# Performance work log

Hardware: AMD Instinct MI355X
Metric: run time of the kernel (lower is better)

Reference implementation:

```python
import jax, jax.numpy as jnp
import numpy as np

CM = 0.05   # collision_margin
NT = 4      # n_timesteps

def _lin(x, W, b):
    return x @ W + b

def _mlp2(x, W1, b1, W2, b2):
    return _lin(jax.nn.relu(_lin(x, W1, b1)), W2, b2)

def _mlp3(x, W1, b1, W2, b2, W3, b3):
    h = jax.nn.relu(_lin(x, W1, b1))
    h = jax.nn.relu(_lin(h, W2, b2))
    return _lin(h, W3, b3)

def _xavier(key, fan_in, fan_out):
    std = np.sqrt(2.0 / (fan_in + fan_out))
    return jax.random.normal(key, (fan_in, fan_out), dtype=jnp.float32) * std

def setup_inputs() -> dict:
    key = jax.random.key(0)
    ks = jax.random.split(key, 16)
    sd, h, es, ud, rd, gd = 8, 128, 128, 32, 64, 32
    B, N, T = 16, 64, 8
    inp = {
        'states': jax.random.normal(ks[0], (B, N, T, sd), dtype=jnp.float32),
        'temp': 1,
        # StateEncoder: Linear(sd,h)-ReLU-Linear(h,es)-ReLU
        'sW1': _xavier(ks[1], sd, h), 'sb1': jnp.zeros((h,), jnp.float32),
        'sW2': _xavier(ks[2], h, es), 'sb2': jnp.zeros((es,), jnp.float32),
        # InputEncoder (collision_margin path): Linear(sd,h)-ReLU-Linear(h,ud)
        'uW1': _xavier(ks[3], sd, h), 'ub1': jnp.zeros((h,), jnp.float32),
        'uW2': _xavier(ks[4], h, ud), 'ub2': jnp.zeros((ud,), jnp.float32),
        # InputPropagator: Linear(es+ud, ud)
        'upW': _xavier(ks[5], es + ud, ud), 'upb': jnp.zeros((ud,), jnp.float32),
        # RelationEncoder (collision_margin path): Linear(sd,h)-ReLU-Linear(h,rd)
        'reW1': _xavier(ks[6], sd, h), 'reb1': jnp.zeros((h,), jnp.float32),
        'reW2': _xavier(ks[7], h, rd), 'reb2': jnp.zeros((rd,), jnp.float32),
        # RelationPropagator: Linear(2*es+rd, rd)
        'rpW': _xavier(ks[8], 2 * es + rd, rd), 'rpb': jnp.zeros((rd,), jnp.float32),
        # ComposedEmbedding: Linear(es+ud+rd,h)-ReLU-Linear(h,h)-ReLU-Linear(h,gd)
        'cW1': _xavier(ks[9], es + ud + rd, h), 'cb1': jnp.zeros((h,), jnp.float32),
        'cW2': _xavier(ks[10], h, h), 'cb2': jnp.zeros((h,), jnp.float32),
        'cW3': _xavier(ks[11], h, gd), 'cb3': jnp.zeros((gd,), jnp.float32),
    }
    return inp

def reference(states, temp, sW1, sb1, sW2, sb2, uW1, ub1, uW2, ub2, upW, upb,
              reW1, reb1, reW2, reb2, rpW, rpb, cW1, cb1, cW2, cb2, cW3, cb3):
    B, N, T, sd = states.shape
    BT = B * T
    s = states.transpose(0, 2, 1, 3).reshape(BT, N, sd)  # [BT,N,sd]

    # node encoders
    enc_obj = jax.nn.relu(_mlp2(s, sW1, sb1, sW2, sb2))   # [BT,N,es]
    enc_u = _mlp2(s, uW1, ub1, uW2, ub2)                  # [BT,N,ud] (no relu in collision_margin path)
    # u mask (get_u_states_mask)
    u = ((jnp.abs(s[..., 0:1]) > 1 - CM) | (jnp.abs(s[..., NT:NT + 1]) > 1 - CM)).astype(s.dtype)

    obs_u = jax.nn.relu(_lin(jnp.concatenate([enc_obj, enc_u], axis=-1), upW, upb))  # [BT,N,ud]
    enc_comp = jnp.concatenate([enc_obj, obs_u], axis=-1)  # [BT,N,es+ud]

    # pairwise relations: receiver i (dim1), sender j (dim2)
    rel_states = s[:, :, None, :] - s[:, None, :, :]        # [BT,N,N,sd]
    enc_rel = jax.nn.relu(_mlp2(rel_states, reW1, reb1, reW2, reb2))  # [BT,N,N,rd]
    sel = ((jnp.abs(rel_states[..., 0:1]) > 2 * CM) |
           (jnp.abs(rel_states[..., NT:NT + 1]) > 2 * CM)).astype(s.dtype)  # [BT,N,N,1]

    es = enc_obj.shape[-1]
    recv = jnp.broadcast_to(enc_obj[:, :, None, :], (BT, N, N, es))
    send = jnp.broadcast_to(enc_obj[:, None, :, :], (BT, N, N, es))
    rel_in = jnp.concatenate([recv, send, enc_rel], axis=-1)            # [BT,N,N,2es+rd]
    rel_eff = jax.nn.relu(_lin(rel_in, rpW, rpb)) * sel                 # [BT,N,N,rd]
    rel_agg = rel_eff.sum(axis=2)                                       # scatter-sum over senders -> [BT,N,rd]

    enc_comp = jnp.concatenate([enc_comp, rel_agg], axis=-1)            # [BT,N,es+ud+rd]
    g = _mlp3(enc_comp, cW1, cb1, cW2, cb2, cW3, cb3)                   # [BT,N,gd]
    return g.reshape(B, T, N, -1)
```

## Files before the change

### kernel.cpp

```cpp
#include <hip/hip_runtime.h>
#include <hip/hip_bf16.h>


typedef __bf16 bf16x8 __attribute__((ext_vector_type(8)));
typedef _Float16 half8 __attribute__((ext_vector_type(8)));
typedef float f32x4 __attribute__((ext_vector_type(4)));

static __device__ __forceinline__ half8 relu8(half8 x) {
    half8 z = {};
    return __builtin_elementwise_max(x, z);
}

__global__ __launch_bounds__(256) void k_prep(
    const float* __restrict__ sW1, const float* __restrict__ uW1,
    const float* __restrict__ reW1, const float* __restrict__ sW2,
    const float* __restrict__ uW2, const float* __restrict__ upW,
    const float* __restrict__ reW2, const float* __restrict__ rpW,
    const float* __restrict__ cW1, const float* __restrict__ cW2,
    const float* __restrict__ cW3,
    __bf16* __restrict__ Wl1f, __bf16* __restrict__ Ws2f,
    __bf16* __restrict__ Wu2f, __bf16* __restrict__ Wupf,
    __bf16* __restrict__ Wabf, _Float16* __restrict__ W2f,
    _Float16* __restrict__ Wbf, __bf16* __restrict__ Wc1f,
    __bf16* __restrict__ Wc2f, __bf16* __restrict__ Wc3f)
{
    const int tid  = blockIdx.x * 256 + threadIdx.x;
    const int nthr = gridDim.x * 256;

#define PACK(dst, CAST, NKT, NCT, EXPR)                             \
    for (int q = tid; q < (NKT) * (NCT) * 512; q += nthr) {         \
        const int f = q >> 9, rem = q & 511;                        \
        const int lane = rem >> 3, e = rem & 7;                     \
        const int kt = f / (NCT), ct = f % (NCT);                   \
        const int k = kt * 32 + (lane >> 4) * 8 + e;                \
        const int c = ct * 16 + (lane & 15);                        \
        (dst)[q] = (CAST)(EXPR);                                    \
        (void)k; (void)c;                                           \
    }

    PACK(Wl1f, __bf16, 1, 24, (k >= 8 ? 0.f :
        (c < 128 ? sW1[k * 128 + c] :
         c < 256 ? uW1[k * 128 + (c - 128)] : reW1[k * 128 + (c - 256)])))
    PACK(Ws2f, __bf16, 4, 8, sW2[k * 128 + c])
    PACK(Wu2f, __bf16, 4, 2, uW2[k * 32 + c])
    PACK(Wupf, __bf16, 5, 2, (k < 160 ? upW[k * 32 + c] : 0.f))
    PACK(Wabf, __bf16, 4, 8, (c < 64 ? rpW[k * 64 + c] : rpW[(128 + k) * 64 + (c - 64)]))
    PACK(W2f,  _Float16, 4, 4, reW2[k * 64 + c])
    PACK(Wbf,  _Float16, 2, 4, rpW[(256 + k) * 64 + c])
    PACK(Wc1f, __bf16, 7, 8, cW1[k * 128 + c])
    PACK(Wc2f, __bf16, 4, 8, cW2[k * 128 + c])
    PACK(Wc3f, __bf16, 4, 2, cW3[k * 32 + c])
#undef PACK
}

__global__ __launch_bounds__(512) void k_node(
    const float* __restrict__ states,
    const float* __restrict__ sb1, const float* __restrict__ sb2,
    const float* __restrict__ ub1, const float* __restrict__ ub2,
    const float* __restrict__ upb,
    const __bf16* __restrict__ Wl1f, const __bf16* __restrict__ Ws2f,
    const __bf16* __restrict__ Wu2f, const __bf16* __restrict__ Wupf,
    const __bf16* __restrict__ Wabf,
    _Float16* __restrict__ P_h, float* __restrict__ A_g,
    _Float16* __restrict__ Bh_g, __bf16* __restrict__ x_g)
{
    const int t = threadIdx.x;
    const int lane = t & 63;
    const int w = t >> 6;
    const int lr = lane >> 4, lc = lane & 15;
    const int nb = blockIdx.x * 16;

    __shared__ __bf16 s_h1hu[16 * 256];
    __shared__ __bf16 s_eoeu[16 * 192];

    bf16x8 af1 = {};
    if (lr == 0) {
        const int rg = nb + lc;
        const int bt = rg >> 6, n = rg & 63;
        const int b = bt >> 3, ts = bt & 7;
        const float* sp = &states[((size_t)((b * 64 + n) * 8 + ts)) * 8];
        const float4 s0 = *reinterpret_cast<const float4*>(sp);
        const float4 s1 = *reinterpret_cast<const float4*>(sp + 4);
        af1[0] = (__bf16)s0.x; af1[1] = (__bf16)s0.y;
        af1[2] = (__bf16)s0.z; af1[3] = (__bf16)s0.w;
        af1[4] = (__bf16)s1.x; af1[5] = (__bf16)s1.y;
        af1[6] = (__bf16)s1.z; af1[7] = (__bf16)s1.w;
    }

    #pragma unroll
    for (int ci = 0; ci < 3; ++ci) {
        const int ct = w * 3 + ci;
        const bf16x8 wf = *reinterpret_cast<const bf16x8*>(
            Wl1f + ((size_t)(ct * 64 + lane)) * 8);
        const float bias = (ct < 8) ? sb1[ct * 16 + lc]
                          : (ct < 16) ? ub1[(ct - 8) * 16 + lc] : 0.f;
        f32x4 acc = {bias, bias, bias, bias};
        acc = __builtin_amdgcn_mfma_f32_16x16x32_bf16(af1, wf, acc, 0, 0, 0);
        #pragma unroll
        for (int r = 0; r < 4; ++r) {
            const int jj = lr * 4 + r;
            if (ct < 16) {
                const int col = ct * 16 + lc;
                const int g = col >> 3;
                s_h1hu[jj * 256 + (((g ^ (jj & 7)) << 3) | (col & 7))] =
                    (__bf16)fmaxf(acc[r], 0.f);
            } else {
                P_h[(size_t)(nb + jj) * 128 + (ct - 16) * 16 + lc] =
                    (_Float16)acc[r];
            }
        }
    }
    __syncthreads();

    const int jr = lc;
    const int sw = lc & 7;
    bf16x8 h1f[4];
    #pragma unroll
    for (int kt = 0; kt < 4; ++kt)
        h1f[kt] = *reinterpret_cast<const bf16x8*>(
            &s_h1hu[jr * 256 + (((kt * 4 + lr) ^ sw) << 3)]);
    {
        const int ct = w;
        const float bias = sb2[ct * 16 + lc];
        f32x4 acc = {bias, bias, bias, bias};
        #pragma unroll
        for (int kt = 0; kt < 4; ++kt) {
            const bf16x8 wf = *reinterpret_cast<const bf16x8*>(
                Ws2f + ((size_t)((kt * 8 + ct) * 64 + lane)) * 8);
            acc = __builtin_amdgcn_mfma_f32_16x16x32_bf16(h1f[kt], wf, acc, 0, 0, 0);
        }
        #pragma unroll
        for (int r = 0; r < 4; ++r) {
            const int jj = lr * 4 + r;
            const int col = ct * 16 + lc;
            const __bf16 v = (__bf16)fmaxf(acc[r], 0.f);
            x_g[(size_t)(nb + jj) * 160 + col] = v;
            const int g = col >> 3;
            s_eoeu[jj * 192 + (((g ^ (jj & 7)) << 3) | (col & 7))] = v;
        }
    }
    if (w < 2) {
        bf16x8 huf[4];
        #pragma unroll
        for (int kt = 0; kt < 4; ++kt)
            huf[kt] = *reinterpret_cast<const bf16x8*>(
                &s_h1hu[jr * 256 + (((16 + kt * 4 + lr) ^ sw) << 3)]);
        const int ct = w;
        const float bias = ub2[ct * 16 + lc];
        f32x4 acc = {bias, bias, bias, bias};
        #pragma unroll
        for (int kt = 0; kt < 4; ++kt) {
            const bf16x8 wf = *reinterpret_cast<const bf16x8*>(
                Wu2f + ((size_t)((kt * 2 + ct) * 64 + lane)) * 8);
            acc = __builtin_amdgcn_mfma_f32_16x16x32_bf16(huf[kt], wf, acc, 0, 0, 0);
        }
        #pragma unroll
        for (int r = 0; r < 4; ++r) {
            const int jj = lr * 4 + r;
            const int col = 128 + ct * 16 + lc;
            const int g = col >> 3;
            s_eoeu[jj * 192 + (((g ^ (jj & 7)) << 3) | (col & 7))] = (__bf16)acc[r];
        }
    }
    __syncthreads();

    bf16x8 eof[5];
    #pragma unroll
    for (int kt = 0; kt < 4; ++kt)
        eof[kt] = *reinterpret_cast<const bf16x8*>(
            &s_eoeu[jr * 192 + (((kt * 4 + lr) ^ sw) << 3)]);
    eof[4] = *reinterpret_cast<const bf16x8*>(
        &s_eoeu[jr * 192 + (((16 + lr) ^ sw) << 3)]);

    if (w >= 6) {
        const int ct = w - 6;
        const float bias = upb[ct * 16 + lc];
        f32x4 acc = {bias, bias, bias, bias};
        #pragma unroll
        for (int kt = 0; kt < 5; ++kt) {
            const bf16x8 wf = *reinterpret_cast<const bf16x8*>(
                Wupf + ((size_t)((kt * 2 + ct) * 64 + lane)) * 8);
            acc = __builtin_amdgcn_mfma_f32_16x16x32_bf16(eof[kt], wf, acc, 0, 0, 0);
        }
        #pragma unroll
        for (int r = 0; r < 4; ++r) {
            const int rg = nb + lr * 4 + r;
            x_g[(size_t)rg * 160 + 128 + ct * 16 + lc] = (__bf16)fmaxf(acc[r], 0.f);
        }
    }
    {
        const int ct = w;
        f32x4 acc = {0.f, 0.f, 0.f, 0.f};
        #pragma unroll
        for (int kt = 0; kt < 4; ++kt) {
            const bf16x8 wf = *reinterpret_cast<const bf16x8*>(
                Wabf + ((size_t)((kt * 8 + ct) * 64 + lane)) * 8);
            acc = __builtin_amdgcn_mfma_f32_16x16x32_bf16(eof[kt], wf, acc, 0, 0, 0);
        }
        #pragma unroll
        for (int r = 0; r < 4; ++r) {
            const int rg = nb + lr * 4 + r;
            if (ct < 4) A_g[(size_t)rg * 64 + ct * 16 + lc] = acc[r];
            else        Bh_g[(size_t)rg * 64 + (ct - 4) * 16 + lc] = (_Float16)acc[r];
        }
    }
}

__global__ __launch_bounds__(512, 2) void k_pairc(
    const float* __restrict__ states,
    const _Float16* __restrict__ P_h, const float* __restrict__ A_g,
    const _Float16* __restrict__ Bh_g, const __bf16* __restrict__ x_g,
    const float* __restrict__ reb1, const float* __restrict__ reb2,
    const float* __restrict__ rpb,
    const _Float16* __restrict__ W2f, const _Float16* __restrict__ Wbf,
    const float* __restrict__ cb1, const float* __restrict__ cb2,
    const float* __restrict__ cb3,
    const __bf16* __restrict__ Wc1f, const __bf16* __restrict__ Wc2f,
    const __bf16* __restrict__ Wc3f,
    float* __restrict__ out)
{
    const int t    = threadIdx.x;
    const int lane = t & 63;
    const int w    = t >> 6;
    const int lr   = lane >> 4;
    const int lc   = lane & 15;
    const int bid  = (blockIdx.x & 7) * 64 + (blockIdx.x >> 3);
    const int bt   = bid >> 2;
    const int ig   = bid & 3;
    const int b    = bt >> 3, tstep = bt & 7;
    const int rowb = bt * 64 + ig * 16;

    __shared__ _Float16 s_pj[64 * 128];
    __shared__ _Float16 s_er[8][16 * 64];
    __shared__ _Float16 s_bm[64 * 72];
    __shared__ float    s_ai[16 * 64];
    __shared__ _Float16 s_rb[128];
    __shared__ float    s_s0[64], s_s4[64];

    for (int idx = t; idx < 1024; idx += 512) {
        const int j = idx >> 4, g = idx & 15;
        const half8 v = *reinterpret_cast<const half8*>(
            P_h + (size_t)(bt * 64 + j) * 128 + g * 8);
        *reinterpret_cast<half8*>(&s_pj[j * 128 + ((g ^ (j & 7)) << 3)]) = v;
    }
    {
        const int j = t >> 3, c8 = (t & 7) * 8;
        if (t < 512)
            *reinterpret_cast<half8*>(&s_bm[j * 72 + c8]) =
                *reinterpret_cast<const half8*>(
                    Bh_g + (size_t)(bt * 64 + j) * 64 + c8);
    }
    for (int idx = t; idx < 1024; idx += 512) {
        const int il = idx >> 6, c = idx & 63;
        s_ai[idx] = A_g[(size_t)(rowb + il) * 64 + c] + rpb[c];
    }
    if (t < 128) s_rb[t] = (_Float16)reb1[t];
    if (t < 64) {
        const float* sp = &states[((size_t)((b * 64 + t) * 8 + tstep)) * 8];
        s_s0[t] = sp[0];
        s_s4[t] = sp[4];
    }

    half8 w2f[4][4];
    #pragma unroll
    for (int kt = 0; kt < 4; ++kt)
        #pragma unroll
        for (int ct = 0; ct < 4; ++ct)
            w2f[kt][ct] = *reinterpret_cast<const half8*>(
                W2f + ((size_t)((kt * 4 + ct) * 64 + lane)) * 8);
    half8 wbf[2][4];
    #pragma unroll
    for (int kt = 0; kt < 2; ++kt)
        #pragma unroll
        for (int ct = 0; ct < 4; ++ct)
            wbf[kt][ct] = *reinterpret_cast<const half8*>(
                Wbf + ((size_t)((kt * 4 + ct) * 64 + lane)) * 8);
    float reb2c[4];
    #pragma unroll
    for (int ct = 0; ct < 4; ++ct) reb2c[ct] = reb2[ct * 16 + lc];

    __syncthreads();

    _Float16* er = s_er[w];
    float rag2[2][4];

    for (int q = 0; q < 2; ++q) {
        const int il = w * 2 + q;
        const int i  = ig * 16 + il;
        const int isw = i & 7;

        half8 pib[4];
        #pragma unroll
        for (int kt = 0; kt < 4; ++kt) {
            const int g = kt * 4 + lr;
            const half8 pv = *reinterpret_cast<const half8*>(
                &s_pj[i * 128 + ((g ^ isw) << 3)]);
            const half8 rb = *reinterpret_cast<const half8*>(&s_rb[g * 8]);
            pib[kt] = pv + rb;
        }
        float aic[4];
        #pragma unroll
        for (int ct = 0; ct < 4; ++ct) aic[ct] = s_ai[il * 64 + ct * 16 + lc];
        const unsigned long long selm = __ballot(
            fabsf(s_s0[i] - s_s0[lane]) > 0.1f ||
            fabsf(s_s4[i] - s_s4[lane]) > 0.1f);

        float ragg[4] = {0.f, 0.f, 0.f, 0.f};

        for (int jt = 0; jt < 4; ++jt) {
            const int j = jt * 16 + lc;
            const int jsw = j & 7;
            half8 af[4];
            #pragma unroll
            for (int kt = 0; kt < 4; ++kt) {
                const int g = (kt * 4 + lr) ^ jsw;
                const half8 pj = *reinterpret_cast<const half8*>(
                    &s_pj[j * 128 + (g << 3)]);
                af[kt] = relu8(pib[kt] - pj);
            }
            #pragma unroll
            for (int ct = 0; ct < 4; ++ct) {
                f32x4 acc = {reb2c[ct], reb2c[ct], reb2c[ct], reb2c[ct]};
                #pragma unroll
                for (int kt = 0; kt < 4; ++kt)
                    acc = __builtin_amdgcn_mfma_f32_16x16x32_f16(
                        af[kt], w2f[kt][ct], acc, 0, 0, 0);
                #pragma unroll
                for (int r = 0; r < 4; ++r) {
                    const int jj2 = lr * 4 + r;
                    const int c = ct * 16 + lc;
                    er[jj2 * 64 + ((((c >> 3) ^ (jj2 & 7)) << 3) | (c & 7))] =
                        (_Float16)fmaxf(acc[r], 0.f);
                }
            }
            half8 a2[2];
            #pragma unroll
            for (int kt = 0; kt < 2; ++kt) {
                const int g = (kt * 4 + lr) ^ (lc & 7);
                a2[kt] = *reinterpret_cast<const half8*>(&er[lc * 64 + (g << 3)]);
            }
            #pragma unroll
            for (int ct = 0; ct < 4; ++ct) {
                f32x4 acc = {aic[ct], aic[ct], aic[ct], aic[ct]};
                #pragma unroll
                for (int kt = 0; kt < 2; ++kt)
                    acc = __builtin_amdgcn_mfma_f32_16x16x32_f16(
                        a2[kt], wbf[kt][ct], acc, 0, 0, 0);
                #pragma unroll
                for (int r = 0; r < 4; ++r) {
                    const int jj = jt * 16 + lr * 4 + r;
                    const float bm = (float)s_bm[jj * 72 + ct * 16 + lc];
                    float v = fmaxf(acc[r] + bm, 0.f);
                    v = ((selm >> jj) & 1ull) ? v : 0.f;
                    ragg[ct] += v;
                }
            }
        }
        #pragma unroll
        for (int ct = 0; ct < 4; ++ct) {
            ragg[ct] += __shfl_xor(ragg[ct], 16);
            ragg[ct] += __shfl_xor(ragg[ct], 32);
            rag2[q][ct] = ragg[ct];
        }
    }
    __syncthreads();

    __bf16* s_x  = reinterpret_cast<__bf16*>(s_pj);
    __bf16* s_h1 = s_x + 16 * 256;
    __bf16* s_h2 = s_h1 + 16 * 128;

    for (int idx = t; idx < 320; idx += 512) {
        const int j = idx / 20, g = idx - j * 20;
        const bf16x8 v = *reinterpret_cast<const bf16x8*>(
            x_g + (size_t)(rowb + j) * 160 + g * 8);
        *reinterpret_cast<bf16x8*>(&s_x[j * 256 + ((g ^ (j & 7)) << 3)]) = v;
    }
    if (lr == 0) {
        #pragma unroll
        for (int q = 0; q < 2; ++q) {
            const int il = w * 2 + q;
            #pragma unroll
            for (int ct = 0; ct < 4; ++ct) {
                const int c = ct * 16 + lc;
                const int gg = 20 + (c >> 3);
                s_x[il * 256 + ((gg ^ (il & 7)) << 3) + (c & 7)] =
                    (__bf16)rag2[q][ct];
            }
        }
    }
    __syncthreads();

    const int jr = lc;
    const int sw = lc & 7;
    bf16x8 xf[7];
    #pragma unroll
    for (int kt = 0; kt < 7; ++kt)
        xf[kt] = *reinterpret_cast<const bf16x8*>(
            &s_x[jr * 256 + (((kt * 4 + lr) ^ sw) << 3)]);
    {
        const int ct = w;
        const float bias = cb1[ct * 16 + lc];
        f32x4 acc = {bias, bias, bias, bias};
        #pragma unroll
        for (int kt = 0; kt < 7; ++kt) {
            const bf16x8 wf = *reinterpret_cast<const bf16x8*>(
                Wc1f + ((size_t)((kt * 8 + ct) * 64 + lane)) * 8);
            acc = __builtin_amdgcn_mfma_f32_16x16x32_bf16(xf[kt], wf, acc, 0, 0, 0);
        }
        #pragma unroll
        for (int r = 0; r < 4; ++r) {
            const int jj = lr * 4 + r;
            const int col = ct * 16 + lc, g = col >> 3;
            s_h1[jj * 128 + (((g ^ (jj & 7)) << 3) | (col & 7))] =
                (__bf16)fmaxf(acc[r], 0.f);
        }
    }
    __syncthreads();

    bf16x8 hf[4];
    #pragma unroll
    for (int kt = 0; kt < 4; ++kt)
        hf[kt] = *reinterpret_cast<const bf16x8*>(
            &s_h1[jr * 128 + (((kt * 4 + lr) ^ sw) << 3)]);
    {
        const int ct = w;
        const float bias = cb2[ct * 16 + lc];
        f32x4 acc = {bias, bias, bias, bias};
        #pragma unroll
        for (int kt = 0; kt < 4; ++kt) {
            const bf16x8 wf = *reinterpret_cast<const bf16x8*>(
                Wc2f + ((size_t)((kt * 8 + ct) * 64 + lane)) * 8);
            acc = __builtin_amdgcn_mfma_f32_16x16x32_bf16(hf[kt], wf, acc, 0, 0, 0);
        }
        #pragma unroll
        for (int r = 0; r < 4; ++r) {
            const int jj = lr * 4 + r;
            const int col = ct * 16 + lc, g = col >> 3;
            s_h2[jj * 128 + (((g ^ (jj & 7)) << 3) | (col & 7))] =
                (__bf16)fmaxf(acc[r], 0.f);
        }
    }
    __syncthreads();

    if (w < 2) {
        bf16x8 h2f[4];
        #pragma unroll
        for (int kt = 0; kt < 4; ++kt)
            h2f[kt] = *reinterpret_cast<const bf16x8*>(
                &s_h2[jr * 128 + (((kt * 4 + lr) ^ sw) << 3)]);
        const int ct = w;
        const float bias = cb3[ct * 16 + lc];
        f32x4 acc = {bias, bias, bias, bias};
        #pragma unroll
        for (int kt = 0; kt < 4; ++kt) {
            const bf16x8 wf = *reinterpret_cast<const bf16x8*>(
                Wc3f + ((size_t)((kt * 2 + ct) * 64 + lane)) * 8);
            acc = __builtin_amdgcn_mfma_f32_16x16x32_bf16(h2f[kt], wf, acc, 0, 0, 0);
        }
        #pragma unroll
        for (int r = 0; r < 4; ++r) {
            const int rg = rowb + lr * 4 + r;
            out[(size_t)rg * 32 + ct * 16 + lc] = acc[r];
        }
    }
}

extern "C" void kernel_launch(void* const* d_in, const int* in_sizes, int n_in,
                              void* d_out, int out_size, void* d_ws, size_t ws_size,
                              hipStream_t stream) {
    const float* states = (const float*)d_in[0];
    const float* sW1  = (const float*)d_in[2];
    const float* sb1  = (const float*)d_in[3];
    const float* sW2  = (const float*)d_in[4];
    const float* sb2  = (const float*)d_in[5];
    const float* uW1  = (const float*)d_in[6];
    const float* ub1  = (const float*)d_in[7];
    const float* uW2  = (const float*)d_in[8];
    const float* ub2  = (const float*)d_in[9];
    const float* upW  = (const float*)d_in[10];
    const float* upb  = (const float*)d_in[11];
    const float* reW1 = (const float*)d_in[12];
    const float* reb1 = (const float*)d_in[13];
    const float* reW2 = (const float*)d_in[14];
    const float* reb2 = (const float*)d_in[15];
    const float* rpW  = (const float*)d_in[16];
    const float* rpb  = (const float*)d_in[17];
    const float* cW1  = (const float*)d_in[18];
    const float* cb1  = (const float*)d_in[19];
    const float* cW2  = (const float*)d_in[20];
    const float* cb2  = (const float*)d_in[21];
    const float* cW3  = (const float*)d_in[22];
    const float* cb3  = (const float*)d_in[23];
    float* out = (float*)d_out;

    float* ws = (float*)d_ws;
    float* A_g = ws;
    _Float16* P_h  = (_Float16*)(A_g + 8192 * 64);
    _Float16* Bh_g = P_h + 8192 * 128;
    _Float16* W2f  = Bh_g + 8192 * 64;
    _Float16* Wbf  = W2f + 16 * 512;
    __bf16* x_g  = (__bf16*)(Wbf + 8 * 512);
    __bf16* Wl1f = x_g + 8192 * 160;
    __bf16* Ws2f = Wl1f + 24 * 512;
    __bf16* Wu2f = Ws2f + 32 * 512;
    __bf16* Wupf = Wu2f + 8 * 512;
    __bf16* Wabf = Wupf + 10 * 512;
    __bf16* Wc1f = Wabf + 32 * 512;
    __bf16* Wc2f = Wc1f + 56 * 512;
    __bf16* Wc3f = Wc2f + 32 * 512;

    k_prep<<<64, 256, 0, stream>>>(sW1, uW1, reW1, sW2, uW2, upW, reW2, rpW,
                                   cW1, cW2, cW3,
                                   Wl1f, Ws2f, Wu2f, Wupf, Wabf, W2f, Wbf,
                                   Wc1f, Wc2f, Wc3f);
    k_node<<<512, 512, 0, stream>>>(states, sb1, sb2, ub1, ub2, upb,
                                    Wl1f, Ws2f, Wu2f, Wupf, Wabf,
                                    P_h, A_g, Bh_g, x_g);
    k_pairc<<<512, 512, 0, stream>>>(states, P_h, A_g, Bh_g, x_g,
                                     reb1, reb2, rpb, W2f, Wbf,
                                     cb1, cb2, cb3, Wc1f, Wc2f, Wc3f, out);
}
```

Measured before the change: 147.2 us.

## Fuse node-encoder kernel into pairwise kernel, recomputing per-timestep node features

Merges k_node into the pairwise/composition kernel. Each block now computes the state encoder, the first relation-layer projection (P) and the sender projection (B) for all 64 nodes of its timestep in shared memory, instead of reading them from global workspace. This removes a kernel launch and the global round trip for P_h, A_g, Bh_g and x_g. The cost is redundant work: each of the four blocks sharing a timestep recomputes the node encoder for all 64 nodes. Shared memory use also rises, which may limit occupancy under launch_bounds(512,2).

```diff
diff --git a/kernel.cpp b/kernel.cpp
--- a/kernel.cpp
+++ b/kernel.cpp
@@ -4,6 +4,7 @@
 
 typedef __bf16 bf16x8 __attribute__((ext_vector_type(8)));
 typedef _Float16 half8 __attribute__((ext_vector_type(8)));
+typedef _Float16 half4 __attribute__((ext_vector_type(4)));
 typedef float f32x4 __attribute__((ext_vector_type(4)));
 
 static __device__ __forceinline__ half8 relu8(half8 x) {
@@ -53,168 +54,18 @@
 #undef PACK
 }
 
-__global__ __launch_bounds__(512) void k_node(
+__global__ __launch_bounds__(512, 2) void k_mega(
     const float* __restrict__ states,
     const float* __restrict__ sb1, const float* __restrict__ sb2,
     const float* __restrict__ ub1, const float* __restrict__ ub2,
-    const float* __restrict__ upb,
+    const float* __restrict__ upb, const float* __restrict__ reb1,
+    const float* __restrict__ reb2, const float* __restrict__ rpb,
+    const float* __restrict__ cb1, const float* __restrict__ cb2,
+    const float* __restrict__ cb3,
     const __bf16* __restrict__ Wl1f, const __bf16* __restrict__ Ws2f,
     const __bf16* __restrict__ Wu2f, const __bf16* __restrict__ Wupf,
     const __bf16* __restrict__ Wabf,
-    _Float16* __restrict__ P_h, float* __restrict__ A_g,
-    _Float16* __restrict__ Bh_g, __bf16* __restrict__ x_g)
-{
-    const int t = threadIdx.x;
-    const int lane = t & 63;
-    const int w = t >> 6;
-    const int lr = lane >> 4, lc = lane & 15;
-    const int nb = blockIdx.x * 16;
-
-    __shared__ __bf16 s_h1hu[16 * 256];
-    __shared__ __bf16 s_eoeu[16 * 192];
-
-    bf16x8 af1 = {};
-    if (lr == 0) {
-        const int rg = nb + lc;
-        const int bt = rg >> 6, n = rg & 63;
-        const int b = bt >> 3, ts = bt & 7;
-        const float* sp = &states[((size_t)((b * 64 + n) * 8 + ts)) * 8];
-        const float4 s0 = *reinterpret_cast<const float4*>(sp);
-        const float4 s1 = *reinterpret_cast<const float4*>(sp + 4);
-        af1[0] = (__bf16)s0.x; af1[1] = (__bf16)s0.y;
-        af1[2] = (__bf16)s0.z; af1[3] = (__bf16)s0.w;
-        af1[4] = (__bf16)s1.x; af1[5] = (__bf16)s1.y;
-        af1[6] = (__bf16)s1.z; af1[7] = (__bf16)s1.w;
-    }
-
-    #pragma unroll
-    for (int ci = 0; ci < 3; ++ci) {
-        const int ct = w * 3 + ci;
-        const bf16x8 wf = *reinterpret_cast<const bf16x8*>(
-            Wl1f + ((size_t)(ct * 64 + lane)) * 8);
-        const float bias = (ct < 8) ? sb1[ct * 16 + lc]
-                          : (ct < 16) ? ub1[(ct - 8) * 16 + lc] : 0.f;
-        f32x4 acc = {bias, bias, bias, bias};
-        acc = __builtin_amdgcn_mfma_f32_16x16x32_bf16(af1, wf, acc, 0, 0, 0);
-        #pragma unroll
-        for (int r = 0; r < 4; ++r) {
-            const int jj = lr * 4 + r;
-            if (ct < 16) {
-                const int col = ct * 16 + lc;
-                const int g = col >> 3;
-                s_h1hu[jj * 256 + (((g ^ (jj & 7)) << 3) | (col & 7))] =
-                    (__bf16)fmaxf(acc[r], 0.f);
-            } else {
-                P_h[(size_t)(nb + jj) * 128 + (ct - 16) * 16 + lc] =
-                    (_Float16)acc[r];
-            }
-        }
-    }
-    __syncthreads();
-
-    const int jr = lc;
-    const int sw = lc & 7;
-    bf16x8 h1f[4];
-    #pragma unroll
-    for (int kt = 0; kt < 4; ++kt)
-        h1f[kt] = *reinterpret_cast<const bf16x8*>(
-            &s_h1hu[jr * 256 + (((kt * 4 + lr) ^ sw) << 3)]);
-    {
-        const int ct = w;
-        const float bias = sb2[ct * 16 + lc];
-        f32x4 acc = {bias, bias, bias, bias};
-        #pragma unroll
-        for (int kt = 0; kt < 4; ++kt) {
-            const bf16x8 wf = *reinterpret_cast<const bf16x8*>(
-                Ws2f + ((size_t)((kt * 8 + ct) * 64 + lane)) * 8);
-            acc = __builtin_amdgcn_mfma_f32_16x16x32_bf16(h1f[kt], wf, acc, 0, 0, 0);
-        }
-        #pragma unroll
-        for (int r = 0; r < 4; ++r) {
-            const int jj = lr * 4 + r;
-            const int col = ct * 16 + lc;
-            const __bf16 v = (__bf16)fmaxf(acc[r], 0.f);
-            x_g[(size_t)(nb + jj) * 160 + col] = v;
-            const int g = col >> 3;
-            s_eoeu[jj * 192 + (((g ^ (jj & 7)) << 3) | (col & 7))] = v;
-        }
-    }
-    if (w < 2) {
-        bf16x8 huf[4];
-        #pragma unroll
-        for (int kt = 0; kt < 4; ++kt)
-            huf[kt] = *reinterpret_cast<const bf16x8*>(
-                &s_h1hu[jr * 256 + (((16 + kt * 4 + lr) ^ sw) << 3)]);
-        const int ct = w;
-        const float bias = ub2[ct * 16 + lc];
-        f32x4 acc = {bias, bias, bias, bias};
-        #pragma unroll
-        for (int kt = 0; kt < 4; ++kt) {
-            const bf16x8 wf = *reinterpret_cast<const bf16x8*>(
-                Wu2f + ((size_t)((kt * 2 + ct) * 64 + lane)) * 8);
-            acc = __builtin_amdgcn_mfma_f32_16x16x32_bf16(huf[kt], wf, acc, 0, 0, 0);
-        }
-        #pragma unroll
-        for (int r = 0; r < 4; ++r) {
-            const int jj = lr * 4 + r;
-            const int col = 128 + ct * 16 + lc;
-            const int g = col >> 3;
-            s_eoeu[jj * 192 + (((g ^ (jj & 7)) << 3) | (col & 7))] = (__bf16)acc[r];
-        }
-    }
-    __syncthreads();
-
-    bf16x8 eof[5];
-    #pragma unroll
-    for (int kt = 0; kt < 4; ++kt)
-        eof[kt] = *reinterpret_cast<const bf16x8*>(
-            &s_eoeu[jr * 192 + (((kt * 4 + lr) ^ sw) << 3)]);
-    eof[4] = *reinterpret_cast<const bf16x8*>(
-        &s_eoeu[jr * 192 + (((16 + lr) ^ sw) << 3)]);
-
-    if (w >= 6) {
-        const int ct = w - 6;
-        const float bias = upb[ct * 16 + lc];
-        f32x4 acc = {bias, bias, bias, bias};
-        #pragma unroll
-        for (int kt = 0; kt < 5; ++kt) {
-            const bf16x8 wf = *reinterpret_cast<const bf16x8*>(
-                Wupf + ((size_t)((kt * 2 + ct) * 64 + lane)) * 8);
-            acc = __builtin_amdgcn_mfma_f32_16x16x32_bf16(eof[kt], wf, acc, 0, 0, 0);
-        }
-        #pragma unroll
-        for (int r = 0; r < 4; ++r) {
-            const int rg = nb + lr * 4 + r;
-            x_g[(size_t)rg * 160 + 128 + ct * 16 + lc] = (__bf16)fmaxf(acc[r], 0.f);
-        }
-    }
-    {
-        const int ct = w;
-        f32x4 acc = {0.f, 0.f, 0.f, 0.f};
-        #pragma unroll
-        for (int kt = 0; kt < 4; ++kt) {
-            const bf16x8 wf = *reinterpret_cast<const bf16x8*>(
-                Wabf + ((size_t)((kt * 8 + ct) * 64 + lane)) * 8);
-            acc = __builtin_amdgcn_mfma_f32_16x16x32_bf16(eof[kt], wf, acc, 0, 0, 0);
-        }
-        #pragma unroll
-        for (int r = 0; r < 4; ++r) {
-            const int rg = nb + lr * 4 + r;
-            if (ct < 4) A_g[(size_t)rg * 64 + ct * 16 + lc] = acc[r];
-            else        Bh_g[(size_t)rg * 64 + (ct - 4) * 16 + lc] = (_Float16)acc[r];
-        }
-    }
-}
-
-__global__ __launch_bounds__(512, 2) void k_pairc(
-    const float* __restrict__ states,
-    const _Float16* __restrict__ P_h, const float* __restrict__ A_g,
-    const _Float16* __restrict__ Bh_g, const __bf16* __restrict__ x_g,
-    const float* __restrict__ reb1, const float* __restrict__ reb2,
-    const float* __restrict__ rpb,
     const _Float16* __restrict__ W2f, const _Float16* __restrict__ Wbf,
-    const float* __restrict__ cb1, const float* __restrict__ cb2,
-    const float* __restrict__ cb3,
     const __bf16* __restrict__ Wc1f, const __bf16* __restrict__ Wc2f,
     const __bf16* __restrict__ Wc3f,
     float* __restrict__ out)
@@ -231,35 +82,182 @@
     const int rowb = bt * 64 + ig * 16;
 
     __shared__ _Float16 s_pj[64 * 128];
-    __shared__ _Float16 s_er[8][16 * 64];
-    __shared__ _Float16 s_bm[64 * 72];
+    __shared__ _Float16 s_bmT[64 * 72];
     __shared__ float    s_ai[16 * 64];
+    __shared__ __bf16   s_eo[64 * 128];
+    __shared__ __bf16   s_scr[16 * 256];
+    __shared__ __bf16   s_x[16 * 256];
+    __shared__ __bf16   s_eu[16 * 40];
     __shared__ _Float16 s_rb[128];
     __shared__ float    s_s0[64], s_s4[64];
 
-    for (int idx = t; idx < 1024; idx += 512) {
-        const int j = idx >> 4, g = idx & 15;
-        const half8 v = *reinterpret_cast<const half8*>(
-            P_h + (size_t)(bt * 64 + j) * 128 + g * 8);
-        *reinterpret_cast<half8*>(&s_pj[j * 128 + ((g ^ (j & 7)) << 3)]) = v;
-    }
-    {
-        const int j = t >> 3, c8 = (t & 7) * 8;
-        if (t < 512)
-            *reinterpret_cast<half8*>(&s_bm[j * 72 + c8]) =
-                *reinterpret_cast<const half8*>(
-                    Bh_g + (size_t)(bt * 64 + j) * 64 + c8);
-    }
-    for (int idx = t; idx < 1024; idx += 512) {
-        const int il = idx >> 6, c = idx & 63;
-        s_ai[idx] = A_g[(size_t)(rowb + il) * 64 + c] + rpb[c];
-    }
     if (t < 128) s_rb[t] = (_Float16)reb1[t];
     if (t < 64) {
         const float* sp = &states[((size_t)((b * 64 + t) * 8 + tstep)) * 8];
         s_s0[t] = sp[0];
         s_s4[t] = sp[4];
     }
+
+    for (int rt = 0; rt < 4; ++rt) {
+        bf16x8 af1 = {};
+        if (lr == 0) {
+            const int n = rt * 16 + lc;
+            const float* sp = &states[((size_t)((b * 64 + n) * 8 + tstep)) * 8];
+            const float4 v0 = *reinterpret_cast<const float4*>(sp);
+            const float4 v1 = *reinterpret_cast<const float4*>(sp + 4);
+            af1[0] = (__bf16)v0.x; af1[1] = (__bf16)v0.y;
+            af1[2] = (__bf16)v0.z; af1[3] = (__bf16)v0.w;
+            af1[4] = (__bf16)v1.x; af1[5] = (__bf16)v1.y;
+            af1[6] = (__bf16)v1.z; af1[7] = (__bf16)v1.w;
+        }
+        const int nct = (rt == ig) ? 3 : 2;
+        for (int ci = 0; ci < nct; ++ci) {
+            const int ct = (ci < 2) ? (w * 2 + ci) : (16 + w);
+            const int wl = (ct < 8) ? ct : (ct < 16 ? ct + 8 : ct - 8);
+            const bf16x8 wf = *reinterpret_cast<const bf16x8*>(
+                Wl1f + ((size_t)(wl * 64 + lane)) * 8);
+            const float bias = (ct < 8) ? sb1[ct * 16 + lc]
+                              : (ct >= 16) ? ub1[(ct - 16) * 16 + lc] : 0.f;
+            f32x4 acc = {bias, bias, bias, bias};
+            acc = __builtin_amdgcn_mfma_f32_16x16x32_bf16(af1, wf, acc, 0, 0, 0);
+            #pragma unroll
+            for (int r = 0; r < 4; ++r) {
+                const int jj = lr * 4 + r;
+                if (ct < 8) {
+                    const int col = ct * 16 + lc, g = col >> 3;
+                    s_scr[jj * 256 + (((g ^ (jj & 7)) << 3) | (col & 7))] =
+                        (__bf16)fmaxf(acc[r], 0.f);
+                } else if (ct < 16) {
+                    const int col = (ct - 8) * 16 + lc, g = col >> 3;
+                    const int j64 = rt * 16 + jj;
+                    s_pj[j64 * 128 + ((g ^ (j64 & 7)) << 3) + (col & 7)] =
+                        (_Float16)acc[r];
+                } else {
+                    const int col = 128 + (ct - 16) * 16 + lc, g = col >> 3;
+                    s_scr[jj * 256 + (((g ^ (jj & 7)) << 3) | (col & 7))] =
+                        (__bf16)fmaxf(acc[r], 0.f);
+                }
+            }
+        }
+        __syncthreads();
+
+        {
+            const int jr = lc, sw = lc & 7;
+            bf16x8 h1f[4];
+            #pragma unroll
+            for (int kt = 0; kt < 4; ++kt)
+                h1f[kt] = *reinterpret_cast<const bf16x8*>(
+                    &s_scr[jr * 256 + (((kt * 4 + lr) ^ sw) << 3)]);
+            const int ct = w;
+            const float bias = sb2[ct * 16 + lc];
+            f32x4 acc = {bias, bias, bias, bias};
+            #pragma unroll
+            for (int kt = 0; kt < 4; ++kt) {
+                const bf16x8 wf = *reinterpret_cast<const bf16x8*>(
+                    Ws2f + ((size_t)((kt * 8 + ct) * 64 + lane)) * 8);
+                acc = __builtin_amdgcn_mfma_f32_16x16x32_bf16(h1f[kt], wf, acc, 0, 0, 0);
+            }
+            #pragma unroll
+            for (int r = 0; r < 4; ++r) {
+                const int jj = lr * 4 + r;
+                const int j64 = rt * 16 + jj;
+                const int col = ct * 16 + lc, g = col >> 3;
+                const __bf16 v = (__bf16)fmaxf(acc[r], 0.f);
+                s_eo[j64 * 128 + (((g ^ (j64 & 7)) << 3) | (col & 7))] = v;
+                if (rt == ig)
+                    s_x[jj * 256 + (((g ^ (jj & 7)) << 3) | (col & 7))] = v;
+            }
+            if (rt == ig && w < 2) {
+                bf16x8 huf[4];
+                #pragma unroll
+                for (int kt = 0; kt < 4; ++kt)
+                    huf[kt] = *reinterpret_cast<const bf16x8*>(
+                        &s_scr[jr * 256 + (((16 + kt * 4 + lr) ^ sw) << 3)]);
+                const float bias2 = ub2[w * 16 + lc];
+                f32x4 acc2 = {bias2, bias2, bias2, bias2};
+                #pragma unroll
+                for (int kt = 0; kt < 4; ++kt) {
+                    const bf16x8 wf = *reinterpret_cast<const bf16x8*>(
+                        Wu2f + ((size_t)((kt * 2 + w) * 64 + lane)) * 8);
+                    acc2 = __builtin_amdgcn_mfma_f32_16x16x32_bf16(huf[kt], wf, acc2, 0, 0, 0);
+                }
+                #pragma unroll
+                for (int r = 0; r < 4; ++r)
+                    s_eu[(lr * 4 + r) * 40 + w * 16 + lc] = (__bf16)acc2[r];
+            }
+        }
+        __syncthreads();
+    }
+
+    {
+        #pragma unroll
+        for (int q = 0; q < 2; ++q) {
+            const int task = w * 2 + q;
+            const int rt2 = task >> 2;
+            const int ct = 4 + (task & 3);
+            const int j64 = rt2 * 16 + lc, so = j64 & 7;
+            bf16x8 eof[4];
+            #pragma unroll
+            for (int kt = 0; kt < 4; ++kt)
+                eof[kt] = *reinterpret_cast<const bf16x8*>(
+                    &s_eo[j64 * 128 + (((kt * 4 + lr) ^ so) << 3)]);
+            f32x4 acc = {0.f, 0.f, 0.f, 0.f};
+            #pragma unroll
+            for (int kt = 0; kt < 4; ++kt) {
+                const bf16x8 wf = *reinterpret_cast<const bf16x8*>(
+                    Wabf + ((size_t)((kt * 8 + ct) * 64 + lane)) * 8);
+                acc = __builtin_amdgcn_mfma_f32_16x16x32_bf16(eof[kt], wf, acc, 0, 0, 0);
+            }
+            #pragma unroll
+            for (int r = 0; r < 4; ++r)
+                s_bmT[((ct - 4) * 16 + lc) * 72 + rt2 * 16 + lr * 4 + r] =
+                    (_Float16)acc[r];
+        }
+        const int jo = ig * 16 + lc, so2 = jo & 7;
+        if (w < 4) {
+            bf16x8 eof[4];
+            #pragma unroll
+            for (int kt = 0; kt < 4; ++kt)
+                eof[kt] = *reinterpret_cast<const bf16x8*>(
+                    &s_eo[jo * 128 + (((kt * 4 + lr) ^ so2) << 3)]);
+            f32x4 acc = {0.f, 0.f, 0.f, 0.f};
+            #pragma unroll
+            for (int kt = 0; kt < 4; ++kt) {
+                const bf16x8 wf = *reinterpret_cast<const bf16x8*>(
+                    Wabf + ((size_t)((kt * 8 + w) * 64 + lane)) * 8);
+                acc = __builtin_amdgcn_mfma_f32_16x16x32_bf16(eof[kt], wf, acc, 0, 0, 0);
+            }
+            #pragma unroll
+            for (int r = 0; r < 4; ++r) {
+                const int col = w * 16 + lc;
+                s_ai[(lr * 4 + r) * 64 + col] = acc[r] + rpb[col];
+            }
+        } else if (w < 6) {
+            const int ct = w - 4;
+            bf16x8 eof[5];
+            #pragma unroll
+            for (int kt = 0; kt < 4; ++kt)
+                eof[kt] = *reinterpret_cast<const bf16x8*>(
+                    &s_eo[jo * 128 + (((kt * 4 + lr) ^ so2) << 3)]);
+            eof[4] = *reinterpret_cast<const bf16x8*>(&s_eu[lc * 40 + lr * 8]);
+            const float bias = upb[ct * 16 + lc];
+            f32x4 acc = {bias, bias, bias, bias};
+            #pragma unroll
+            for (int kt = 0; kt < 5; ++kt) {
+                const bf16x8 wf = *reinterpret_cast<const bf16x8*>(
+                    Wupf + ((size_t)((kt * 2 + ct) * 64 + lane)) * 8);
+                acc = __builtin_amdgcn_mfma_f32_16x16x32_bf16(eof[kt], wf, acc, 0, 0, 0);
+            }
+            #pragma unroll
+            for (int r = 0; r < 4; ++r) {
+                const int jj = lr * 4 + r;
+                const int col = 128 + ct * 16 + lc, g = col >> 3;
+                s_x[jj * 256 + (((g ^ (jj & 7)) << 3) | (col & 7))] =
+                    (__bf16)fmaxf(acc[r], 0.f);
+            }
+        }
+    }
+    __syncthreads();
 
     half8 w2f[4][4];
     #pragma unroll
@@ -279,9 +277,7 @@
     #pragma unroll
     for (int ct = 0; ct < 4; ++ct) reb2c[ct] = reb2[ct * 16 + lc];
 
-    __syncthreads();
-
-    _Float16* er = s_er[w];
+    _Float16* er = reinterpret_cast<_Float16*>(s_eo) + w * (16 * 64);
     float rag2[2][4];
 
     for (int q = 0; q < 2; ++q) {
@@ -341,7 +337,10 @@
             }
             #pragma unroll
             for (int ct = 0; ct < 4; ++ct) {
-                f32x4 acc = {aic[ct], aic[ct], aic[ct], aic[ct]};
+                const half4 bm4 = *reinterpret_cast<const half4*>(
+                    &s_bmT[(ct * 16 + lc) * 72 + jt * 16 + lr * 4]);
+                f32x4 acc = {aic[ct] + (float)bm4[0], aic[ct] + (float)bm4[1],
+                             aic[ct] + (float)bm4[2], aic[ct] + (float)bm4[3]};
                 #pragma unroll
                 for (int kt = 0; kt < 2; ++kt)
                     acc = __builtin_amdgcn_mfma_f32_16x16x32_f16(
@@ -349,8 +348,7 @@
                 #pragma unroll
                 for (int r = 0; r < 4; ++r) {
                     const int jj = jt * 16 + lr * 4 + r;
-                    const float bm = (float)s_bm[jj * 72 + ct * 16 + lc];
-                    float v = fmaxf(acc[r] + bm, 0.f);
+                    float v = fmaxf(acc[r], 0.f);
                     v = ((selm >> jj) & 1ull) ? v : 0.f;
                     ragg[ct] += v;
                 }
@@ -362,18 +360,6 @@
             ragg[ct] += __shfl_xor(ragg[ct], 32);
             rag2[q][ct] = ragg[ct];
         }
-    }
-    __syncthreads();
-
-    __bf16* s_x  = reinterpret_cast<__bf16*>(s_pj);
-    __bf16* s_h1 = s_x + 16 * 256;
-    __bf16* s_h2 = s_h1 + 16 * 128;
-
-    for (int idx = t; idx < 320; idx += 512) {
-        const int j = idx / 20, g = idx - j * 20;
-        const bf16x8 v = *reinterpret_cast<const bf16x8*>(
-            x_g + (size_t)(rowb + j) * 160 + g * 8);
-        *reinterpret_cast<bf16x8*>(&s_x[j * 256 + ((g ^ (j & 7)) << 3)]) = v;
     }
     if (lr == 0) {
         #pragma unroll
@@ -389,6 +375,9 @@
         }
     }
     __syncthreads();
+
+    __bf16* s_h1 = s_scr;
+    __bf16* s_h2 = s_scr + 16 * 128;
 
     const int jr = lc;
     const int sw = lc & 7;
@@ -417,12 +406,12 @@
     }
     __syncthreads();
 
-    bf16x8 hf[4];
-    #pragma unroll
-    for (int kt = 0; kt < 4; ++kt)
-        hf[kt] = *reinterpret_cast<const bf16x8*>(
-            &s_h1[jr * 128 + (((kt * 4 + lr) ^ sw) << 3)]);
     {
+        bf16x8 hf[4];
+        #pragma unroll
+        for (int kt = 0; kt < 4; ++kt)
+            hf[kt] = *reinterpret_cast<const bf16x8*>(
+                &s_h1[jr * 128 + (((kt * 4 + lr) ^ sw) << 3)]);
         const int ct = w;
         const float bias = cb2[ct * 16 + lc];
         f32x4 acc = {bias, bias, bias, bias};
@@ -493,14 +482,9 @@
     const float* cb3  = (const float*)d_in[23];
     float* out = (float*)d_out;
 
-    float* ws = (float*)d_ws;
-    float* A_g = ws;
-    _Float16* P_h  = (_Float16*)(A_g + 8192 * 64);
-    _Float16* Bh_g = P_h + 8192 * 128;
-    _Float16* W2f  = Bh_g + 8192 * 64;
+    _Float16* W2f  = (_Float16*)d_ws;
     _Float16* Wbf  = W2f + 16 * 512;
-    __bf16* x_g  = (__bf16*)(Wbf + 8 * 512);
-    __bf16* Wl1f = x_g + 8192 * 160;
+    __bf16* Wl1f = (__bf16*)(Wbf + 8 * 512);
     __bf16* Ws2f = Wl1f + 24 * 512;
     __bf16* Wu2f = Ws2f + 32 * 512;
     __bf16* Wupf = Wu2f + 8 * 512;
@@ -513,10 +497,8 @@
                                    cW1, cW2, cW3,
                                    Wl1f, Ws2f, Wu2f, Wupf, Wabf, W2f, Wbf,
                                    Wc1f, Wc2f, Wc3f);
-    k_node<<<512, 512, 0, stream>>>(states, sb1, sb2, ub1, ub2, upb,
-                                    Wl1f, Ws2f, Wu2f, Wupf, Wabf,
-                                    P_h, A_g, Bh_g, x_g);
-    k_pairc<<<512, 512, 0, stream>>>(states, P_h, A_g, Bh_g, x_g,
-                                     reb1, reb2, rpb, W2f, Wbf,
-                                     cb1, cb2, cb3, Wc1f, Wc2f, Wc3f, out);
+    k_mega<<<512, 512, 0, stream>>>(states, sb1, sb2, ub1, ub2, upb,
+                                    reb1, reb2, rpb, cb1, cb2, cb3,
+                                    Wl1f, Ws2f, Wu2f, Wupf, Wabf, W2f, Wbf,
+                                    Wc1f, Wc2f, Wc3f, out);
 }
```

Result: slower. 152.2 us (+3.4%).
